# Performance work log

Measured on AMD Instinct MI355X. Metric: run time of the kernel, lower is better.

The kernel has to match this reference:

```python
import jax, jax.numpy as jnp
import numpy as np

DIM = 192
HEADS = 6
HSP = 8
WSP = 8
POS_DIM = (DIM // 4) // 4  # 12


def _ln(x, g, b, eps=1e-5):
    m = jnp.mean(x, -1, keepdims=True)
    v = jnp.mean((x - m) ** 2, -1, keepdims=True)
    return (x - m) / jnp.sqrt(v + eps) * g + b


def _rel_tables():
    # rpe_biases: ((2*HSP-1)*(2*WSP-1), 2) float coords of all relative offsets
    bh, bw = np.meshgrid(np.arange(1 - HSP, HSP), np.arange(1 - WSP, WSP), indexing='ij')
    biases = np.stack([bh, bw], -1).reshape(-1, 2).astype(np.float32)
    # relative_position_index: (N, N) int lookup into the bias table
    ch, cw = np.meshgrid(np.arange(HSP), np.arange(WSP), indexing='ij')
    coords = np.stack([ch, cw], 0).reshape(2, -1)  # (2, N)
    rel = coords[:, :, None] - coords[:, None, :]  # (2, N, N)
    idx = (rel[0] + HSP - 1) * (2 * WSP - 1) + (rel[1] + WSP - 1)
    return jnp.asarray(biases), jnp.asarray(idx.astype(np.int32))


def setup_inputs() -> dict:
    key = jax.random.key(0)
    ks = jax.random.split(key, 8)
    B, H, W = 2, 256, 256
    L = H * W
    def lin(k, i, o):
        return jax.random.normal(k, (i, o), jnp.float32) * 0.02
    return {
        'qkv': jax.random.normal(ks[0], (3, B, L, DIM), jnp.float32),
        'w_proj': lin(ks[1], 2, POS_DIM), 'b_proj': jnp.zeros((POS_DIM,), jnp.float32),
        'g1': jnp.ones((POS_DIM,), jnp.float32), 'be1': jnp.zeros((POS_DIM,), jnp.float32),
        'w1': lin(ks[2], POS_DIM, POS_DIM), 'b1': jnp.zeros((POS_DIM,), jnp.float32),
        'g2': jnp.ones((POS_DIM,), jnp.float32), 'be2': jnp.zeros((POS_DIM,), jnp.float32),
        'w2': lin(ks[3], POS_DIM, POS_DIM), 'b2': jnp.zeros((POS_DIM,), jnp.float32),
        'g3': jnp.ones((POS_DIM,), jnp.float32), 'be3': jnp.zeros((POS_DIM,), jnp.float32),
        'w3': lin(ks[4], POS_DIM, HEADS), 'b3': jnp.zeros((HEADS,), jnp.float32),
        'H': H, 'W': W,
    }


def reference(qkv, w_proj, b_proj, g1, be1, w1, b1, g2, be2, w2, b2, g3, be3, w3, b3, H, W):
    B, L, C = qkv.shape[1], qkv.shape[2], qkv.shape[3]
    hd = C // HEADS
    scale = float(hd) ** -0.5
    N = HSP * WSP

    def im2win(x):
        # (B, L, C) -> (B*nW, heads, N, hd)
        x = x.reshape(B, H // HSP, HSP, W // WSP, WSP, C)
        x = x.transpose(0, 1, 3, 2, 4, 5).reshape(-1, N, HEADS, hd)
        return x.transpose(0, 2, 1, 3)

    q = im2win(qkv[0]) * scale
    k = im2win(qkv[1])
    v = im2win(qkv[2])

    attn = jnp.einsum('whnd,whmd->whnm', q, k)  # (B*nW, heads, N, N)

    # dynamic relative position bias via MLP (DynamicPosBias, residual=False)
    biases, rel_idx = _rel_tables()
    p = biases @ w_proj + b_proj
    p = jax.nn.relu(_ln(p, g1, be1)) @ w1 + b1
    p = jax.nn.relu(_ln(p, g2, be2)) @ w2 + b2
    p = jax.nn.relu(_ln(p, g3, be3)) @ w3 + b3  # (n_rel, heads)
    rpb = p[rel_idx.reshape(-1)].reshape(N, N, HEADS).transpose(2, 0, 1)  # (heads, N, N)
    attn = attn + rpb[None]

    attn = jax.nn.softmax(attn, axis=-1)
    x = jnp.einsum('whnm,whmd->whnd', attn, v)  # (B*nW, heads, N, hd)
    x = x.transpose(0, 2, 1, 3).reshape(-1, N, C)

    # windows2img: (B*nW, N, C) -> (B, H, W, C)
    x = x.reshape(B, H // HSP, W // WSP, HSP, WSP, C)
    x = x.transpose(0, 1, 3, 2, 4, 5).reshape(B, H, W, C)
    return x
```

## Files before the change

kernel.cpp:

```cpp
#include <hip/hip_runtime.h>
#include <hip/hip_bf16.h>

#define NHEADS 6
#define HD 32
#define CDIM 192
#define NTOK 64
#define NREL 225
#define PDIM 12
#define IMG 256
#define NWW 32
#define NWIN 2048
#define SCALE 0.17677669529663687f
#define INV_SCALE 5.656854249492381f

typedef __attribute__((ext_vector_type(8))) short v8s;
typedef __attribute__((ext_vector_type(4))) float v4f;

#define QKS 40
#define VTS 72
#define PTS 72

__device__ __forceinline__ unsigned pkbf(float x, float y) {
    __hip_bfloat162 h = __float22bfloat162_rn(make_float2(x, y));
    union { __hip_bfloat162 h; unsigned u; } c; c.h = h;
    return c.u;
}

__device__ __forceinline__ void ln_relu12(const float* x, const float* g,
                                          const float* be, float* y) {
    float m = 0.f;
#pragma unroll
    for (int i = 0; i < PDIM; ++i) m += x[i];
    m *= (1.f / PDIM);
    float v = 0.f;
#pragma unroll
    for (int i = 0; i < PDIM; ++i) { float d = x[i] - m; v += d * d; }
    v *= (1.f / PDIM);
    float inv = rsqrtf(v + 1e-5f);
#pragma unroll
    for (int i = 0; i < PDIM; ++i) {
        float t = (x[i] - m) * inv * g[i] + be[i];
        y[i] = t > 0.f ? t : 0.f;
    }
}

__global__ __launch_bounds__(256) void posbias_kernel(
    const float* __restrict__ wp, const float* __restrict__ bp,
    const float* __restrict__ g1, const float* __restrict__ be1,
    const float* __restrict__ w1, const float* __restrict__ b1,
    const float* __restrict__ g2, const float* __restrict__ be2,
    const float* __restrict__ w2, const float* __restrict__ b2,
    const float* __restrict__ g3, const float* __restrict__ be3,
    const float* __restrict__ w3, const float* __restrict__ b3,
    float* __restrict__ p_t)
{
    int r = threadIdx.x;
    if (r >= NREL) return;
    float x0 = (float)(r / 15 - 7);
    float x1 = (float)(r % 15 - 7);
    float h[PDIM], y[PDIM];
#pragma unroll
    for (int o = 0; o < PDIM; ++o)
        h[o] = x0 * wp[o] + x1 * wp[PDIM + o] + bp[o];
    ln_relu12(h, g1, be1, y);
#pragma unroll
    for (int o = 0; o < PDIM; ++o) {
        float a = b1[o];
#pragma unroll
        for (int i = 0; i < PDIM; ++i) a += y[i] * w1[i * PDIM + o];
        h[o] = a;
    }
    ln_relu12(h, g2, be2, y);
#pragma unroll
    for (int o = 0; o < PDIM; ++o) {
        float a = b2[o];
#pragma unroll
        for (int i = 0; i < PDIM; ++i) a += y[i] * w2[i * PDIM + o];
        h[o] = a;
    }
    ln_relu12(h, g3, be3, y);
#pragma unroll
    for (int o = 0; o < NHEADS; ++o) {
        float a = b3[o];
#pragma unroll
        for (int i = 0; i < PDIM; ++i) a += y[i] * w3[i * NHEADS + o];
        p_t[o * NREL + r] = a * INV_SCALE;
    }
}

__global__ __launch_bounds__(256) void win_attn_mfma(
    const float* __restrict__ qkv, const float* __restrict__ p_t,
    float* __restrict__ out)
{
    __shared__ __align__(16) unsigned short ks[NTOK * QKS];
    __shared__ __align__(16) unsigned short vt[HD * VTS];
    __shared__ __align__(16) unsigned short pt[NTOK * PTS];
    __shared__ float psh[NREL];

    const int t = threadIdx.x;
    const int head = blockIdx.x >> 11;
    const int win  = blockIdx.x & (NWIN - 1);
    const int b    = win >> 10;
    const int bh   = (win >> 5) & 31;
    const int bw   = win & 31;

    const int lane = t & 63;
    const int wave = t >> 6;
    const int lw = lane & 15;
    const int lg = lane >> 4;
    const int rowbase = wave * 16;

    const size_t SST = (size_t)2 * IMG * IMG * CDIM;
    const float* basep = qkv + (size_t)b * IMG * IMG * CDIM + head * HD;

    auto toff = [&](int tok) -> size_t {
        return ((size_t)(bh * 8 + (tok >> 3)) * IMG + (bw * 8 + (tok & 7))) * CDIM;
    };

    float pshv = 0.f;
    if (t < NREL) pshv = p_t[head * NREL + t];

    const int tokK = t >> 3;
    const int dK   = (t & 7) * 4;
    float4 k40 = *(const float4*)(basep + SST + toff(tokK) + dK);
    float4 k41 = *(const float4*)(basep + SST + toff(tokK + 32) + dK);

    const int u  = t & 31;
    const int dg = t >> 5;
    const int ta = (u & 15) + (u >> 4) * 32;
    const int db = dg * 4;
    float4 va  = *(const float4*)(basep + 2 * SST + toff(ta) + db);
    float4 vb4 = *(const float4*)(basep + 2 * SST + toff(ta + 16) + db);

    const float* qp = basep + toff(rowbase + lw) + lg * 8;
    float4 q0 = *(const float4*)qp;
    float4 q1 = *(const float4*)(qp + 4);

    if (t < NREL) psh[t] = pshv;

    uint2 kk0; kk0.x = pkbf(k40.x, k40.y); kk0.y = pkbf(k40.z, k40.w);
    uint2 kk1; kk1.x = pkbf(k41.x, k41.y); kk1.y = pkbf(k41.z, k41.w);
    *(uint2*)&ks[tokK * QKS + dK] = kk0;
    *(uint2*)&ks[(tokK + 32) * QKS + dK] = kk1;

    const int kpa = (u & 15) * 4 + (u >> 4) * 2;
    *(unsigned*)&vt[(db + 0) * VTS + kpa] = pkbf(va.x, vb4.x);
    *(unsigned*)&vt[(db + 1) * VTS + kpa] = pkbf(va.y, vb4.y);
    *(unsigned*)&vt[(db + 2) * VTS + kpa] = pkbf(va.z, vb4.z);
    *(unsigned*)&vt[(db + 3) * VTS + kpa] = pkbf(va.w, vb4.w);

    v8s a;
    {
        union { v8s v; unsigned x[4]; } au;
        au.x[0] = pkbf(q0.x, q0.y);
        au.x[1] = pkbf(q0.z, q0.w);
        au.x[2] = pkbf(q1.x, q1.y);
        au.x[3] = pkbf(q1.z, q1.w);
        a = au.v;
    }
    __syncthreads();

    v4f acc[4];
#pragma unroll
    for (int ct = 0; ct < 4; ++ct) {
        v4f z = {0.f, 0.f, 0.f, 0.f};
        v8s bfr = *(const v8s*)&ks[(ct * 16 + lw) * QKS + lg * 8];
        acc[ct] = __builtin_amdgcn_mfma_f32_16x16x32_bf16(a, bfr, z, 0, 0, 0);
    }

    v4f rinv;
    {
        int base_r[4];
#pragma unroll
        for (int r = 0; r < 4; ++r) {
            int n = rowbase + lg * 4 + r;
            base_r[r] = ((n >> 3) - (lw >> 3) + 7) * 15 + (n & 7) - (lw & 7) + 7;
        }
        v4f s4 = {0.f, 0.f, 0.f, 0.f};
#pragma unroll
        for (int ct = 0; ct < 4; ++ct)
#pragma unroll
            for (int r = 0; r < 4; ++r) {
                float e = __expf((acc[ct][r] + psh[base_r[r] - ct * 30]) * SCALE);
                acc[ct][r] = e;
                s4[r] += e;
            }
#pragma unroll
        for (int off = 1; off < 16; off <<= 1)
#pragma unroll
            for (int r = 0; r < 4; ++r)
                s4[r] += __shfl_xor(s4[r], off);
#pragma unroll
        for (int r = 0; r < 4; ++r) rinv[r] = __builtin_amdgcn_rcpf(s4[r]);
#pragma unroll
        for (int r = 0; r < 4; ++r) {
            uint2 w;
            w.x = pkbf(acc[0][r], acc[1][r]);
            w.y = pkbf(acc[2][r], acc[3][r]);
            *(uint2*)&pt[(rowbase + lg * 4 + r) * PTS + lw * 4] = w;
        }
    }

    {
        v8s pa[2];
#pragma unroll
        for (int kt = 0; kt < 2; ++kt)
            pa[kt] = *(const v8s*)&pt[(rowbase + lw) * PTS + kt * 32 + lg * 8];
        v4f acc2[2] = {};
#pragma unroll
        for (int dt = 0; dt < 2; ++dt)
#pragma unroll
            for (int kt = 0; kt < 2; ++kt) {
                v8s vb = *(const v8s*)&vt[(dt * 16 + lw) * VTS + kt * 32 + lg * 8];
                acc2[dt] = __builtin_amdgcn_mfma_f32_16x16x32_bf16(pa[kt], vb, acc2[dt], 0, 0, 0);
            }
#pragma unroll
        for (int dt = 0; dt < 2; ++dt)
#pragma unroll
            for (int r = 0; r < 4; ++r) {
                int n = rowbase + lg * 4 + r;
                size_t off = (((size_t)b * IMG + bh * 8 + (n >> 3)) * IMG
                              + (bw * 8 + (n & 7))) * CDIM + head * HD + dt * 16 + lw;
                out[off] = acc2[dt][r] * rinv[r];
            }
    }
}

extern "C" void kernel_launch(void* const* d_in, const int* in_sizes, int n_in,
                              void* d_out, int out_size, void* d_ws, size_t ws_size,
                              hipStream_t stream) {
    const float* qkv = (const float*)d_in[0];
    const float* wp  = (const float*)d_in[1];
    const float* bp  = (const float*)d_in[2];
    const float* g1  = (const float*)d_in[3];
    const float* be1 = (const float*)d_in[4];
    const float* w1  = (const float*)d_in[5];
    const float* b1  = (const float*)d_in[6];
    const float* g2  = (const float*)d_in[7];
    const float* be2 = (const float*)d_in[8];
    const float* w2  = (const float*)d_in[9];
    const float* b2  = (const float*)d_in[10];
    const float* g3  = (const float*)d_in[11];
    const float* be3 = (const float*)d_in[12];
    const float* w3  = (const float*)d_in[13];
    const float* b3  = (const float*)d_in[14];

    float* p_t = (float*)d_ws;
    posbias_kernel<<<1, 256, 0, stream>>>(wp, bp, g1, be1, w1, b1,
                                          g2, be2, w2, b2, g3, be3, w3, b3, p_t);
    win_attn_mfma<<<NWIN * NHEADS, 256, 0, stream>>>(qkv, p_t, (float*)d_out);
}
```

Before: 98.09 us.

## Fuse position-bias MLP into attention and process all heads per window block

Removes the separate single-block position-bias kernel and has every attention block recompute the small MLP for all six heads into shared memory. The grid goes from one block per (window, head) to one block per window. Each block loads full 192-channel K and V rows for its window into larger LDS tiles with contiguous pixel reads, then loops over the six heads. This saves a kernel launch and the dependency between the two kernels, and makes global loads more contiguous. In exchange there are 6x fewer blocks, more LDS per block (lower occupancy), more Q registers, and redundant MLP work in every block.

```diff
diff --git a/kernel.cpp b/kernel.cpp
--- a/kernel.cpp
+++ b/kernel.cpp
@@ -8,7 +8,6 @@
 #define NREL 225
 #define PDIM 12
 #define IMG 256
-#define NWW 32
 #define NWIN 2048
 #define SCALE 0.17677669529663687f
 #define INV_SCALE 5.656854249492381f
@@ -16,7 +15,7 @@
 typedef __attribute__((ext_vector_type(8))) short v8s;
 typedef __attribute__((ext_vector_type(4))) float v4f;
 
-#define QKS 40
+#define KS2 200
 #define VTS 72
 #define PTS 72
 
@@ -44,7 +43,8 @@
     }
 }
 
-__global__ __launch_bounds__(256) void posbias_kernel(
+__global__ __launch_bounds__(256) void win_attn_fused(
+    const float* __restrict__ qkv,
     const float* __restrict__ wp, const float* __restrict__ bp,
     const float* __restrict__ g1, const float* __restrict__ be1,
     const float* __restrict__ w1, const float* __restrict__ b1,
@@ -52,57 +52,18 @@
     const float* __restrict__ w2, const float* __restrict__ b2,
     const float* __restrict__ g3, const float* __restrict__ be3,
     const float* __restrict__ w3, const float* __restrict__ b3,
-    float* __restrict__ p_t)
-{
-    int r = threadIdx.x;
-    if (r >= NREL) return;
-    float x0 = (float)(r / 15 - 7);
-    float x1 = (float)(r % 15 - 7);
-    float h[PDIM], y[PDIM];
-#pragma unroll
-    for (int o = 0; o < PDIM; ++o)
-        h[o] = x0 * wp[o] + x1 * wp[PDIM + o] + bp[o];
-    ln_relu12(h, g1, be1, y);
-#pragma unroll
-    for (int o = 0; o < PDIM; ++o) {
-        float a = b1[o];
-#pragma unroll
-        for (int i = 0; i < PDIM; ++i) a += y[i] * w1[i * PDIM + o];
-        h[o] = a;
-    }
-    ln_relu12(h, g2, be2, y);
-#pragma unroll
-    for (int o = 0; o < PDIM; ++o) {
-        float a = b2[o];
-#pragma unroll
-        for (int i = 0; i < PDIM; ++i) a += y[i] * w2[i * PDIM + o];
-        h[o] = a;
-    }
-    ln_relu12(h, g3, be3, y);
-#pragma unroll
-    for (int o = 0; o < NHEADS; ++o) {
-        float a = b3[o];
-#pragma unroll
-        for (int i = 0; i < PDIM; ++i) a += y[i] * w3[i * NHEADS + o];
-        p_t[o * NREL + r] = a * INV_SCALE;
-    }
-}
-
-__global__ __launch_bounds__(256) void win_attn_mfma(
-    const float* __restrict__ qkv, const float* __restrict__ p_t,
     float* __restrict__ out)
 {
-    __shared__ __align__(16) unsigned short ks[NTOK * QKS];
-    __shared__ __align__(16) unsigned short vt[HD * VTS];
+    __shared__ __align__(16) unsigned short ks[NTOK * KS2];
+    __shared__ __align__(16) unsigned short vt[CDIM * VTS];
     __shared__ __align__(16) unsigned short pt[NTOK * PTS];
-    __shared__ float psh[NREL];
+    __shared__ float psh[NHEADS * NREL];
 
     const int t = threadIdx.x;
-    const int head = blockIdx.x >> 11;
-    const int win  = blockIdx.x & (NWIN - 1);
-    const int b    = win >> 10;
-    const int bh   = (win >> 5) & 31;
-    const int bw   = win & 31;
+    const int win = blockIdx.x;
+    const int b  = win >> 10;
+    const int bh = (win >> 5) & 31;
+    const int bw = win & 31;
 
     const int lane = t & 63;
     const int wave = t >> 6;
@@ -110,78 +71,124 @@
     const int lg = lane >> 4;
     const int rowbase = wave * 16;
 
-    const size_t SST = (size_t)2 * IMG * IMG * CDIM;
-    const float* basep = qkv + (size_t)b * IMG * IMG * CDIM + head * HD;
-
-    auto toff = [&](int tok) -> size_t {
+    const size_t PL = (size_t)2 * IMG * IMG * CDIM;
+    const float* qplane = qkv + (size_t)b * IMG * IMG * CDIM;
+    const float* kplane = qplane + PL;
+    const float* vplane = kplane + PL;
+
+    auto pixoff = [&](int tok) -> size_t {
         return ((size_t)(bh * 8 + (tok >> 3)) * IMG + (bw * 8 + (tok & 7))) * CDIM;
     };
 
-    float pshv = 0.f;
-    if (t < NREL) pshv = p_t[head * NREL + t];
-
-    const int tokK = t >> 3;
-    const int dK   = (t & 7) * 4;
-    float4 k40 = *(const float4*)(basep + SST + toff(tokK) + dK);
-    float4 k41 = *(const float4*)(basep + SST + toff(tokK + 32) + dK);
-
-    const int u  = t & 31;
-    const int dg = t >> 5;
-    const int ta = (u & 15) + (u >> 4) * 32;
-    const int db = dg * 4;
-    float4 va  = *(const float4*)(basep + 2 * SST + toff(ta) + db);
-    float4 vb4 = *(const float4*)(basep + 2 * SST + toff(ta + 16) + db);
-
-    const float* qp = basep + toff(rowbase + lw) + lg * 8;
-    float4 q0 = *(const float4*)qp;
-    float4 q1 = *(const float4*)(qp + 4);
-
-    if (t < NREL) psh[t] = pshv;
-
-    uint2 kk0; kk0.x = pkbf(k40.x, k40.y); kk0.y = pkbf(k40.z, k40.w);
-    uint2 kk1; kk1.x = pkbf(k41.x, k41.y); kk1.y = pkbf(k41.z, k41.w);
-    *(uint2*)&ks[tokK * QKS + dK] = kk0;
-    *(uint2*)&ks[(tokK + 32) * QKS + dK] = kk1;
-
-    const int kpa = (u & 15) * 4 + (u >> 4) * 2;
-    *(unsigned*)&vt[(db + 0) * VTS + kpa] = pkbf(va.x, vb4.x);
-    *(unsigned*)&vt[(db + 1) * VTS + kpa] = pkbf(va.y, vb4.y);
-    *(unsigned*)&vt[(db + 2) * VTS + kpa] = pkbf(va.z, vb4.z);
-    *(unsigned*)&vt[(db + 3) * VTS + kpa] = pkbf(va.w, vb4.w);
-
-    v8s a;
+#pragma unroll
+    for (int pass = 0; pass < 12; ++pass) {
+        int fidx = t + pass * 256;
+        int s   = fidx / 384;
+        int rem = fidx - s * 384;
+        int j1  = rem / 48;
+        int f   = rem - j1 * 48;
+        float4 k4 = *(const float4*)(kplane
+                     + ((size_t)(bh * 8 + s) * IMG + (bw * 8 + j1)) * CDIM + f * 4);
+        uint2 kk; kk.x = pkbf(k4.x, k4.y); kk.y = pkbf(k4.z, k4.w);
+        *(uint2*)&ks[(s * 8 + j1) * KS2 + f * 4] = kk;
+    }
+
     {
-        union { v8s v; unsigned x[4]; } au;
-        au.x[0] = pkbf(q0.x, q0.y);
-        au.x[1] = pkbf(q0.z, q0.w);
-        au.x[2] = pkbf(q1.x, q1.y);
-        au.x[3] = pkbf(q1.z, q1.w);
-        a = au.v;
+        const int u  = t & 31;
+        const int dg = t >> 5;
+        const int ta = (u & 15) + (u >> 4) * 32;
+        const int db = dg * 4;
+        const int kpa = (u & 15) * 4 + (u >> 4) * 2;
+        const size_t offa = pixoff(ta), offb = pixoff(ta + 16);
+#pragma unroll
+        for (int h = 0; h < NHEADS; ++h) {
+            float4 va = *(const float4*)(vplane + offa + h * HD + db);
+            float4 vb = *(const float4*)(vplane + offb + h * HD + db);
+            int row = h * HD + db;
+            *(unsigned*)&vt[(row + 0) * VTS + kpa] = pkbf(va.x, vb.x);
+            *(unsigned*)&vt[(row + 1) * VTS + kpa] = pkbf(va.y, vb.y);
+            *(unsigned*)&vt[(row + 2) * VTS + kpa] = pkbf(va.z, vb.z);
+            *(unsigned*)&vt[(row + 3) * VTS + kpa] = pkbf(va.w, vb.w);
+        }
+    }
+
+    v8s aq[NHEADS];
+    {
+        const size_t qoff = pixoff(rowbase + lw);
+#pragma unroll
+        for (int h = 0; h < NHEADS; ++h) {
+            const float* qp = qplane + qoff + h * HD + lg * 8;
+            float4 q0 = *(const float4*)qp;
+            float4 q1 = *(const float4*)(qp + 4);
+            union { v8s v; unsigned x[4]; } au;
+            au.x[0] = pkbf(q0.x, q0.y);
+            au.x[1] = pkbf(q0.z, q0.w);
+            au.x[2] = pkbf(q1.x, q1.y);
+            au.x[3] = pkbf(q1.z, q1.w);
+            aq[h] = au.v;
+        }
+    }
+
+    if (t < NREL) {
+        float x0 = (float)(t / 15 - 7);
+        float x1 = (float)(t % 15 - 7);
+        float h[PDIM], y[PDIM];
+#pragma unroll
+        for (int o = 0; o < PDIM; ++o)
+            h[o] = x0 * wp[o] + x1 * wp[PDIM + o] + bp[o];
+        ln_relu12(h, g1, be1, y);
+#pragma unroll
+        for (int o = 0; o < PDIM; ++o) {
+            float a = b1[o];
+#pragma unroll
+            for (int i = 0; i < PDIM; ++i) a += y[i] * w1[i * PDIM + o];
+            h[o] = a;
+        }
+        ln_relu12(h, g2, be2, y);
+#pragma unroll
+        for (int o = 0; o < PDIM; ++o) {
+            float a = b2[o];
+#pragma unroll
+            for (int i = 0; i < PDIM; ++i) a += y[i] * w2[i * PDIM + o];
+            h[o] = a;
+        }
+        ln_relu12(h, g3, be3, y);
+#pragma unroll
+        for (int o = 0; o < NHEADS; ++o) {
+            float a = b3[o];
+#pragma unroll
+            for (int i = 0; i < PDIM; ++i) a += y[i] * w3[i * NHEADS + o];
+            psh[o * NREL + t] = a * INV_SCALE;
+        }
     }
     __syncthreads();
 
-    v4f acc[4];
-#pragma unroll
-    for (int ct = 0; ct < 4; ++ct) {
-        v4f z = {0.f, 0.f, 0.f, 0.f};
-        v8s bfr = *(const v8s*)&ks[(ct * 16 + lw) * QKS + lg * 8];
-        acc[ct] = __builtin_amdgcn_mfma_f32_16x16x32_bf16(a, bfr, z, 0, 0, 0);
-    }
-
-    v4f rinv;
-    {
-        int base_r[4];
-#pragma unroll
-        for (int r = 0; r < 4; ++r) {
-            int n = rowbase + lg * 4 + r;
-            base_r[r] = ((n >> 3) - (lw >> 3) + 7) * 15 + (n & 7) - (lw & 7) + 7;
-        }
+    int base_r[4];
+    size_t ooff[4];
+#pragma unroll
+    for (int r = 0; r < 4; ++r) {
+        int n = rowbase + lg * 4 + r;
+        base_r[r] = ((n >> 3) - (lw >> 3) + 7) * 15 + (n & 7) - (lw & 7) + 7;
+        ooff[r] = ((size_t)(b * IMG + bh * 8 + (n >> 3)) * IMG
+                   + (bw * 8 + (n & 7))) * CDIM;
+    }
+
+#pragma unroll
+    for (int h = 0; h < NHEADS; ++h) {
+        v4f acc[4];
+#pragma unroll
+        for (int ct = 0; ct < 4; ++ct) {
+            v4f z = {0.f, 0.f, 0.f, 0.f};
+            v8s bfr = *(const v8s*)&ks[(ct * 16 + lw) * KS2 + h * HD + lg * 8];
+            acc[ct] = __builtin_amdgcn_mfma_f32_16x16x32_bf16(aq[h], bfr, z, 0, 0, 0);
+        }
+        const float* ph = &psh[h * NREL];
         v4f s4 = {0.f, 0.f, 0.f, 0.f};
 #pragma unroll
         for (int ct = 0; ct < 4; ++ct)
 #pragma unroll
             for (int r = 0; r < 4; ++r) {
-                float e = __expf((acc[ct][r] + psh[base_r[r] - ct * 30]) * SCALE);
+                float e = __expf((acc[ct][r] + ph[base_r[r] - ct * 30]) * SCALE);
                 acc[ct][r] = e;
                 s4[r] += e;
             }
@@ -190,6 +197,7 @@
 #pragma unroll
             for (int r = 0; r < 4; ++r)
                 s4[r] += __shfl_xor(s4[r], off);
+        v4f rinv;
 #pragma unroll
         for (int r = 0; r < 4; ++r) rinv[r] = __builtin_amdgcn_rcpf(s4[r]);
 #pragma unroll
@@ -199,9 +207,6 @@
             w.y = pkbf(acc[2][r], acc[3][r]);
             *(uint2*)&pt[(rowbase + lg * 4 + r) * PTS + lw * 4] = w;
         }
-    }
-
-    {
         v8s pa[2];
 #pragma unroll
         for (int kt = 0; kt < 2; ++kt)
@@ -211,18 +216,15 @@
         for (int dt = 0; dt < 2; ++dt)
 #pragma unroll
             for (int kt = 0; kt < 2; ++kt) {
-                v8s vb = *(const v8s*)&vt[(dt * 16 + lw) * VTS + kt * 32 + lg * 8];
+                v8s vb = *(const v8s*)&vt[(h * HD + dt * 16 + lw) * VTS
+                                          + kt * 32 + lg * 8];
                 acc2[dt] = __builtin_amdgcn_mfma_f32_16x16x32_bf16(pa[kt], vb, acc2[dt], 0, 0, 0);
             }
 #pragma unroll
         for (int dt = 0; dt < 2; ++dt)
 #pragma unroll
-            for (int r = 0; r < 4; ++r) {
-                int n = rowbase + lg * 4 + r;
-                size_t off = (((size_t)b * IMG + bh * 8 + (n >> 3)) * IMG
-                              + (bw * 8 + (n & 7))) * CDIM + head * HD + dt * 16 + lw;
-                out[off] = acc2[dt][r] * rinv[r];
-            }
+            for (int r = 0; r < 4; ++r)
+                out[ooff[r] + h * HD + dt * 16 + lw] = acc2[dt][r] * rinv[r];
     }
 }
 
@@ -230,23 +232,14 @@
                               void* d_out, int out_size, void* d_ws, size_t ws_size,
                               hipStream_t stream) {
     const float* qkv = (const float*)d_in[0];
-    const float* wp  = (const float*)d_in[1];
-    const float* bp  = (const float*)d_in[2];
-    const float* g1  = (const float*)d_in[3];
-    const float* be1 = (const float*)d_in[4];
-    const float* w1  = (const float*)d_in[5];
-    const float* b1  = (const float*)d_in[6];
-    const float* g2  = (const float*)d_in[7];
-    const float* be2 = (const float*)d_in[8];
-    const float* w2  = (const float*)d_in[9];
-    const float* b2  = (const float*)d_in[10];
-    const float* g3  = (const float*)d_in[11];
-    const float* be3 = (const float*)d_in[12];
-    const float* w3  = (const float*)d_in[13];
-    const float* b3  = (const float*)d_in[14];
-
-    float* p_t = (float*)d_ws;
-    posbias_kernel<<<1, 256, 0, stream>>>(wp, bp, g1, be1, w1, b1,
-                                          g2, be2, w2, b2, g3, be3, w3, b3, p_t);
-    win_attn_mfma<<<NWIN * NHEADS, 256, 0, stream>>>(qkv, p_t, (float*)d_out);
-}
+    win_attn_fused<<<NWIN, 256, 0, stream>>>(
+        qkv,
+        (const float*)d_in[1], (const float*)d_in[2],
+        (const float*)d_in[3], (const float*)d_in[4],
+        (const float*)d_in[5], (const float*)d_in[6],
+        (const float*)d_in[7], (const float*)d_in[8],
+        (const float*)d_in[9], (const float*)d_in[10],
+        (const float*)d_in[11], (const float*)d_in[12],
+        (const float*)d_in[13], (const float*)d_in[14],
+        (float*)d_out);
+}
```

Result: faster. 92.45 us (-5.8%).
